# Kernel optimization log

Hardware: AMD Instinct MI355X
Metric: run time of the kernel (lower is better)

The kernel has to match this reference:

```python
import jax, jax.numpy as jnp
import numpy as np

KH, KW = 2, 2

def setup_inputs() -> dict:
    key = jax.random.key(0)
    k1, k2 = jax.random.split(key)
    x = jax.random.normal(k1, (64, 32, 32, 32), dtype=jnp.float32)
    # logits = log(rand) in torch; emulate with log of uniform to keep same distribution family
    logits = jnp.log(jax.random.uniform(k2, (32, 32, 32, 32), dtype=jnp.float32, minval=1e-6, maxval=1.0))
    return {"x": x, "logits": logits}


def reference(x, logits):
    # SumLayer: log_softmax over in_channels (dim=1), broadcast add, logsumexp over in
    log_w = jax.nn.log_softmax(logits, axis=1)            # [O, I, H, W]
    # x: [N, I, H, W] -> [N, 1, I, H, W]; log_w -> [1, O, I, H, W]
    y = jax.scipy.special.logsumexp(x[:, None] + log_w[None], axis=2)  # [N, O, H, W]
    # ProdConv: grouped conv with ones kernel, stride (KH,KW) == non-overlapping sum-pool
    N, C, H, W = y.shape
    y = y.reshape(N, C, H // KH, KH, W // KW, KW).sum(axis=(3, 5))     # [N, O, H/KH, W/KW]
    return y
```

## Files before the change

### kernel.cpp

```cpp
#include <hip/hip_runtime.h>

namespace {
constexpr int IC = 32;
constexpr int OC = 32;
constexpr int HW = 1024;
constexpr int H2 = 16, W2 = 16;

typedef _Float16 half2v __attribute__((ext_vector_type(2)));

#if defined(__has_builtin)
#if __has_builtin(__builtin_amdgcn_fdot2)
#define HAVE_FDOT2 1
#endif
#endif

__device__ __forceinline__ float dot2acc(half2v a, half2v b, float c) {
#ifdef HAVE_FDOT2
    return __builtin_amdgcn_fdot2(a, b, c, false);
#else
    return fmaf((float)a.x, (float)b.x, fmaf((float)a.y, (float)b.y, c));
#endif
}

__device__ __forceinline__ half2v u2h(unsigned int u) {
    union { unsigned int u; half2v h; } x; x.u = u; return x.h;
}

__device__ __forceinline__ half2v pk2(float a, float b) {
    union { decltype(__builtin_amdgcn_cvt_pkrtz(0.f, 0.f)) p; half2v h; } x;
    x.p = __builtin_amdgcn_cvt_pkrtz(a, b);
    return x.h;
}
}

__global__ __launch_bounds__(512, 4) void sumprod_fused(
    const float* __restrict__ x, const float* __restrict__ logits,
    float* __restrict__ out)
{
    __shared__ half2v exl[8 * 64 * 16];
    __shared__ half2v ewl[8 * 64 * 16];

    const int tid  = threadIdx.x;
    const int lane = tid & 63;
    const int w    = tid >> 6;
    const int bid  = blockIdx.x;
    const int s    = bid & 15;
    const int tt   = bid >> 4;
    const int n0   = (tt & 7) * 8;
    const int o0   = (tt >> 3) * 8;

    const int kk    = (tid >> 4) & 3;
    const int p4    = tid & 15;
    const int spoff = (2 * s + (p4 >> 3)) * 32 + (p4 & 7) * 4;

    const float* gx = x      + (size_t)(n0 + w) * IC * HW + spoff;
    const float* gw = logits + (size_t)(o0 + w) * IC * HW + spoff;

    auto stage = [&](half2v* buf, const float4& va, const float4& vb, int ip) {
        const float* pa = reinterpret_cast<const float*>(&va);
        const float* pb = reinterpret_cast<const float*>(&vb);
        #pragma unroll
        for (int j = 0; j < 4; ++j) {
            const int p    = (p4 >> 3) * 32 + (p4 & 7) * 4 + j;
            const int slot = (ip >> 2) ^ (((p >> 1) ^ (p >> 3)) & 3);
            buf[(w * 64 + p) * 16 + slot * 4 + (ip & 3)] =
                pk2(__expf(pa[j]), __expf(pb[j]));
        }
    };

    #pragma unroll
    for (int g = 0; g < 4; ++g) {
        const int ip = g * 4 + kk;
        const float4 va = *reinterpret_cast<const float4*>(&gw[(2 * ip) * HW]);
        const float4 vb = *reinterpret_cast<const float4*>(&gw[(2 * ip + 1) * HW]);
        stage(ewl, va, vb, ip);
    }
    #pragma unroll
    for (int g = 0; g < 4; ++g) {
        const int ip = g * 4 + kk;
        const float4 va = *reinterpret_cast<const float4*>(&gx[(2 * ip) * HW]);
        const float4 vb = *reinterpret_cast<const float4*>(&gx[(2 * ip + 1) * HW]);
        stage(exl, va, vb, ip);
    }
    __syncthreads();

    const int swl = ((lane >> 1) ^ (lane >> 3)) & 3;
    const int nw = (w & 1) * 4;
    const int ow = (w >> 1) * 2;

    const half2v one2 = {(_Float16)1.f, (_Float16)1.f};
    float den[2];
    #pragma unroll
    for (int j = 0; j < 2; ++j) {
        float ds = 0.f;
        const half2v* rb = &ewl[((ow + j) * 64 + lane) * 16];
        #pragma unroll
        for (int gg = 0; gg < 4; ++gg) {
            const uint4 B = *reinterpret_cast<const uint4*>(rb + ((gg ^ swl) * 4));
            ds = dot2acc(u2h(B.x), one2, ds);
            ds = dot2acc(u2h(B.y), one2, ds);
            ds = dot2acc(u2h(B.z), one2, ds);
            ds = dot2acc(u2h(B.w), one2, ds);
        }
        den[j] = ds;
    }

    float acc[4][2] = {};

#define D2(AA, BB, K, J) acc[K][J] = dot2acc(u2h(AA), u2h(BB), acc[K][J])
#define QUAD(A_, K_)                                                          \
    D2(A_.x, B0.x, K_, 0); D2(A_.y, B0.y, K_, 0);                             \
    D2(A_.z, B0.z, K_, 0); D2(A_.w, B0.w, K_, 0);                             \
    D2(A_.x, B1.x, K_, 1); D2(A_.y, B1.y, K_, 1);                             \
    D2(A_.z, B1.z, K_, 1); D2(A_.w, B1.w, K_, 1)
#define COMPUTE_GG(GG) {                                                      \
    const int off = ((GG) ^ swl) * 4;                                         \
    const uint4 A0 = *reinterpret_cast<const uint4*>(&exl[((nw + 0) * 64 + lane) * 16 + off]); \
    const uint4 A1 = *reinterpret_cast<const uint4*>(&exl[((nw + 1) * 64 + lane) * 16 + off]); \
    const uint4 A2 = *reinterpret_cast<const uint4*>(&exl[((nw + 2) * 64 + lane) * 16 + off]); \
    const uint4 A3 = *reinterpret_cast<const uint4*>(&exl[((nw + 3) * 64 + lane) * 16 + off]); \
    const uint4 B0 = *reinterpret_cast<const uint4*>(&ewl[((ow + 0) * 64 + lane) * 16 + off]); \
    const uint4 B1 = *reinterpret_cast<const uint4*>(&ewl[((ow + 1) * 64 + lane) * 16 + off]); \
    QUAD(A0, 0); QUAD(A1, 1); QUAD(A2, 2); QUAD(A3, 3); }

    COMPUTE_GG(0);
    COMPUTE_GG(1);
    COMPUTE_GG(2);
    COMPUTE_GG(3);

#undef COMPUTE_GG
#undef QUAD
#undef D2

    float dp0 = den[0];
    dp0 *= __shfl_xor(dp0, 1);  dp0 *= __shfl_xor(dp0, 32);
    float dp1 = den[1];
    dp1 *= __shfl_xor(dp1, 1);  dp1 *= __shfl_xor(dp1, 32);

    #pragma unroll
    for (int k = 0; k < 4; ++k) {
        #pragma unroll
        for (int j = 0; j < 2; ++j) {
            float v = acc[k][j];
            v *= __shfl_xor(v, 1);
            v *= __shfl_xor(v, 32);
            if ((lane & 33) == 0) {
                const int w2 = (lane >> 1) & 15;
                out[((n0 + nw + k) * OC + (o0 + ow + j)) * (H2 * W2) + s * W2 + w2] =
                    __logf(v) - __logf(j ? dp1 : dp0);
            }
        }
    }
}

extern "C" void kernel_launch(void* const* d_in, const int* in_sizes, int n_in,
                              void* d_out, int out_size, void* d_ws, size_t ws_size,
                              hipStream_t stream) {
    const float* x      = (const float*)d_in[0];
    const float* logits = (const float*)d_in[1];
    float* out = (float*)d_out;
    hipLaunchKernelGGL(sumprod_fused, dim3(512), dim3(512), 0, stream,
                       x, logits, out);
}
```

Baseline: 13.45 us.

## Halve block size, pipeline x staging across compute, compute denominators in fp32

```diff
diff --git a/kernel.cpp b/kernel.cpp
--- a/kernel.cpp
+++ b/kernel.cpp
@@ -26,23 +26,24 @@
     union { unsigned int u; half2v h; } x; x.u = u; return x.h;
 }
 
-__device__ __forceinline__ half2v pk2(float a, float b) {
-    union { decltype(__builtin_amdgcn_cvt_pkrtz(0.f, 0.f)) p; half2v h; } x;
+__device__ __forceinline__ unsigned int pk2u(float a, float b) {
+    union { decltype(__builtin_amdgcn_cvt_pkrtz(0.f, 0.f)) p; unsigned int u; } x;
     x.p = __builtin_amdgcn_cvt_pkrtz(a, b);
-    return x.h;
-}
-}
-
-__global__ __launch_bounds__(512, 4) void sumprod_fused(
+    return x.u;
+}
+}
+
+__global__ __launch_bounds__(256, 2) void sumprod_fused(
     const float* __restrict__ x, const float* __restrict__ logits,
     float* __restrict__ out)
 {
     __shared__ half2v exl[8 * 64 * 16];
     __shared__ half2v ewl[8 * 64 * 16];
+    __shared__ __align__(16) float wsl[8 * 64];
 
     const int tid  = threadIdx.x;
     const int lane = tid & 63;
-    const int w    = tid >> 6;
+    const int v    = tid >> 6;
     const int bid  = blockIdx.x;
     const int s    = bid & 15;
     const int tt   = bid >> 4;
@@ -51,68 +52,98 @@
 
     const int kk    = (tid >> 4) & 3;
     const int p4    = tid & 15;
-    const int spoff = (2 * s + (p4 >> 3)) * 32 + (p4 & 7) * 4;
-
-    const float* gx = x      + (size_t)(n0 + w) * IC * HW + spoff;
-    const float* gw = logits + (size_t)(o0 + w) * IC * HW + spoff;
-
-    auto stage = [&](half2v* buf, const float4& va, const float4& vb, int ip) {
-        const float* pa = reinterpret_cast<const float*>(&va);
-        const float* pb = reinterpret_cast<const float*>(&vb);
-        #pragma unroll
-        for (int j = 0; j < 4; ++j) {
-            const int p    = (p4 >> 3) * 32 + (p4 & 7) * 4 + j;
-            const int slot = (ip >> 2) ^ (((p >> 1) ^ (p >> 3)) & 3);
-            buf[(w * 64 + p) * 16 + slot * 4 + (ip & 3)] =
-                pk2(__expf(pa[j]), __expf(pb[j]));
-        }
-    };
-
-    #pragma unroll
-    for (int g = 0; g < 4; ++g) {
-        const int ip = g * 4 + kk;
-        const float4 va = *reinterpret_cast<const float4*>(&gw[(2 * ip) * HW]);
-        const float4 vb = *reinterpret_cast<const float4*>(&gw[(2 * ip + 1) * HW]);
-        stage(ewl, va, vb, ip);
-    }
-    #pragma unroll
-    for (int g = 0; g < 4; ++g) {
-        const int ip = g * 4 + kk;
-        const float4 va = *reinterpret_cast<const float4*>(&gx[(2 * ip) * HW]);
-        const float4 vb = *reinterpret_cast<const float4*>(&gx[(2 * ip + 1) * HW]);
-        stage(exl, va, vb, ip);
+    const int pbase = (p4 >> 3) * 32 + (p4 & 7) * 4;
+    const int spoff = 2 * s * 32 + pbase;
+
+    float dsum[2][4] = {};
+    #pragma unroll
+    for (int rr = 0; rr < 2; ++rr) {
+        const int r = v + rr * 4;
+        const float* g = logits + (size_t)(o0 + r) * IC * HW + spoff;
+        float4 va[4], vb[4];
+        #pragma unroll
+        for (int gi = 0; gi < 4; ++gi) {
+            const int ip = kk * 4 + gi;
+            va[gi] = *reinterpret_cast<const float4*>(&g[(2 * ip) * HW]);
+            vb[gi] = *reinterpret_cast<const float4*>(&g[(2 * ip + 1) * HW]);
+        }
+        #pragma unroll
+        for (int j = 0; j < 4; ++j) {
+            const int p    = pbase + j;
+            const int slot = kk ^ (((p >> 1) ^ (p >> 3)) & 3);
+            uint4 wv;
+            unsigned int* wp = &wv.x;
+            #pragma unroll
+            for (int gi = 0; gi < 4; ++gi) {
+                const float ea = __expf(reinterpret_cast<const float*>(&va[gi])[j]);
+                const float eb = __expf(reinterpret_cast<const float*>(&vb[gi])[j]);
+                dsum[rr][j] += ea + eb;
+                wp[gi] = pk2u(ea, eb);
+            }
+            *reinterpret_cast<uint4*>(&ewl[(r * 64 + p) * 16 + slot * 4]) = wv;
+        }
+    }
+    #pragma unroll
+    for (int rr = 0; rr < 2; ++rr) {
+        #pragma unroll
+        for (int j = 0; j < 4; ++j) {
+            float d = dsum[rr][j];
+            d += __shfl_xor(d, 16);
+            d += __shfl_xor(d, 32);
+            dsum[rr][j] = d;
+        }
+        if (kk == 0) {
+            float4 dv = make_float4(dsum[rr][0], dsum[rr][1], dsum[rr][2], dsum[rr][3]);
+            *reinterpret_cast<float4*>(&wsl[(v + rr * 4) * 64 + pbase]) = dv;
+        }
+    }
+
+    const float* gx0 = x + (size_t)(n0 + v) * IC * HW + spoff;
+    const float* gx1 = x + (size_t)(n0 + v + 4) * IC * HW + spoff;
+    #pragma unroll
+    for (int rr = 0; rr < 2; ++rr) {
+        const int r = v + rr * 4;
+        const float* gxr = rr ? gx1 : gx0;
+        float4 a0 = *reinterpret_cast<const float4*>(&gxr[(4 * kk + 0) * HW]);
+        float4 b0 = *reinterpret_cast<const float4*>(&gxr[(4 * kk + 1) * HW]);
+        float4 a1 = *reinterpret_cast<const float4*>(&gxr[(4 * kk + 2) * HW]);
+        float4 b1 = *reinterpret_cast<const float4*>(&gxr[(4 * kk + 3) * HW]);
+        #pragma unroll
+        for (int j = 0; j < 4; ++j) {
+            const int p    = pbase + j;
+            const int slot = (kk >> 1) ^ (((p >> 1) ^ (p >> 3)) & 3);
+            uint2 wv;
+            wv.x = pk2u(__expf(reinterpret_cast<const float*>(&a0)[j]),
+                        __expf(reinterpret_cast<const float*>(&b0)[j]));
+            wv.y = pk2u(__expf(reinterpret_cast<const float*>(&a1)[j]),
+                        __expf(reinterpret_cast<const float*>(&b1)[j]));
+            *reinterpret_cast<uint2*>(
+                &exl[(r * 64 + p) * 16 + slot * 4 + (kk & 1) * 2]) = wv;
+        }
     }
     __syncthreads();
 
+    float4 pf[2][4];
+    #pragma unroll
+    for (int rr = 0; rr < 2; ++rr) {
+        const float* gxr = rr ? gx1 : gx0;
+        pf[rr][0] = *reinterpret_cast<const float4*>(&gxr[(16 + 4 * kk + 0) * HW]);
+        pf[rr][1] = *reinterpret_cast<const float4*>(&gxr[(16 + 4 * kk + 1) * HW]);
+        pf[rr][2] = *reinterpret_cast<const float4*>(&gxr[(16 + 4 * kk + 2) * HW]);
+        pf[rr][3] = *reinterpret_cast<const float4*>(&gxr[(16 + 4 * kk + 3) * HW]);
+    }
+
     const int swl = ((lane >> 1) ^ (lane >> 3)) & 3;
-    const int nw = (w & 1) * 4;
-    const int ow = (w >> 1) * 2;
-
-    const half2v one2 = {(_Float16)1.f, (_Float16)1.f};
-    float den[2];
-    #pragma unroll
-    for (int j = 0; j < 2; ++j) {
-        float ds = 0.f;
-        const half2v* rb = &ewl[((ow + j) * 64 + lane) * 16];
-        #pragma unroll
-        for (int gg = 0; gg < 4; ++gg) {
-            const uint4 B = *reinterpret_cast<const uint4*>(rb + ((gg ^ swl) * 4));
-            ds = dot2acc(u2h(B.x), one2, ds);
-            ds = dot2acc(u2h(B.y), one2, ds);
-            ds = dot2acc(u2h(B.z), one2, ds);
-            ds = dot2acc(u2h(B.w), one2, ds);
-        }
-        den[j] = ds;
-    }
-
-    float acc[4][2] = {};
+    const int nw = (v & 1) * 4;
+    const int ow = (v >> 1) * 4;
+    float acc[4][4] = {};
 
 #define D2(AA, BB, K, J) acc[K][J] = dot2acc(u2h(AA), u2h(BB), acc[K][J])
-#define QUAD(A_, K_)                                                          \
-    D2(A_.x, B0.x, K_, 0); D2(A_.y, B0.y, K_, 0);                             \
-    D2(A_.z, B0.z, K_, 0); D2(A_.w, B0.w, K_, 0);                             \
-    D2(A_.x, B1.x, K_, 1); D2(A_.y, B1.y, K_, 1);                             \
-    D2(A_.z, B1.z, K_, 1); D2(A_.w, B1.w, K_, 1)
+#define OCT(A_, K_)                                                           \
+    D2(A_.x, B0.x, K_, 0); D2(A_.y, B0.y, K_, 0); D2(A_.z, B0.z, K_, 0); D2(A_.w, B0.w, K_, 0); \
+    D2(A_.x, B1.x, K_, 1); D2(A_.y, B1.y, K_, 1); D2(A_.z, B1.z, K_, 1); D2(A_.w, B1.w, K_, 1); \
+    D2(A_.x, B2.x, K_, 2); D2(A_.y, B2.y, K_, 2); D2(A_.z, B2.z, K_, 2); D2(A_.w, B2.w, K_, 2); \
+    D2(A_.x, B3.x, K_, 3); D2(A_.y, B3.y, K_, 3); D2(A_.z, B3.z, K_, 3); D2(A_.w, B3.w, K_, 3)
 #define COMPUTE_GG(GG) {                                                      \
     const int off = ((GG) ^ swl) * 4;                                         \
     const uint4 A0 = *reinterpret_cast<const uint4*>(&exl[((nw + 0) * 64 + lane) * 16 + off]); \
@@ -121,33 +152,53 @@
     const uint4 A3 = *reinterpret_cast<const uint4*>(&exl[((nw + 3) * 64 + lane) * 16 + off]); \
     const uint4 B0 = *reinterpret_cast<const uint4*>(&ewl[((ow + 0) * 64 + lane) * 16 + off]); \
     const uint4 B1 = *reinterpret_cast<const uint4*>(&ewl[((ow + 1) * 64 + lane) * 16 + off]); \
-    QUAD(A0, 0); QUAD(A1, 1); QUAD(A2, 2); QUAD(A3, 3); }
+    const uint4 B2 = *reinterpret_cast<const uint4*>(&ewl[((ow + 2) * 64 + lane) * 16 + off]); \
+    const uint4 B3 = *reinterpret_cast<const uint4*>(&ewl[((ow + 3) * 64 + lane) * 16 + off]); \
+    OCT(A0, 0); OCT(A1, 1); OCT(A2, 2); OCT(A3, 3); }
 
     COMPUTE_GG(0);
     COMPUTE_GG(1);
+
+    #pragma unroll
+    for (int rr = 0; rr < 2; ++rr) {
+        const int r = v + rr * 4;
+        #pragma unroll
+        for (int j = 0; j < 4; ++j) {
+            const int p    = pbase + j;
+            const int slot = (2 + (kk >> 1)) ^ (((p >> 1) ^ (p >> 3)) & 3);
+            uint2 wv;
+            wv.x = pk2u(__expf(reinterpret_cast<const float*>(&pf[rr][0])[j]),
+                        __expf(reinterpret_cast<const float*>(&pf[rr][1])[j]));
+            wv.y = pk2u(__expf(reinterpret_cast<const float*>(&pf[rr][2])[j]),
+                        __expf(reinterpret_cast<const float*>(&pf[rr][3])[j]));
+            *reinterpret_cast<uint2*>(
+                &exl[(r * 64 + p) * 16 + slot * 4 + (kk & 1) * 2]) = wv;
+        }
+    }
+    __syncthreads();
+
     COMPUTE_GG(2);
     COMPUTE_GG(3);
 
 #undef COMPUTE_GG
-#undef QUAD
+#undef OCT
 #undef D2
 
-    float dp0 = den[0];
-    dp0 *= __shfl_xor(dp0, 1);  dp0 *= __shfl_xor(dp0, 32);
-    float dp1 = den[1];
-    dp1 *= __shfl_xor(dp1, 1);  dp1 *= __shfl_xor(dp1, 32);
+    float lw[4];
+    #pragma unroll
+    for (int jj = 0; jj < 4; ++jj)
+        lw[jj] = __logf(wsl[(ow + jj) * 64 + lane]);
 
     #pragma unroll
     for (int k = 0; k < 4; ++k) {
         #pragma unroll
-        for (int j = 0; j < 2; ++j) {
-            float v = acc[k][j];
-            v *= __shfl_xor(v, 1);
-            v *= __shfl_xor(v, 32);
+        for (int jj = 0; jj < 4; ++jj) {
+            float val = __logf(acc[k][jj]) - lw[jj];
+            val += __shfl_xor(val, 1);
+            val += __shfl_xor(val, 32);
             if ((lane & 33) == 0) {
                 const int w2 = (lane >> 1) & 15;
-                out[((n0 + nw + k) * OC + (o0 + ow + j)) * (H2 * W2) + s * W2 + w2] =
-                    __logf(v) - __logf(j ? dp1 : dp0);
+                out[((n0 + nw + k) * OC + (o0 + ow + jj)) * (H2 * W2) + s * W2 + w2] = val;
             }
         }
     }
@@ -159,6 +210,6 @@
     const float* x      = (const float*)d_in[0];
     const float* logits = (const float*)d_in[1];
     float* out = (float*)d_out;
-    hipLaunchKernelGGL(sumprod_fused, dim3(512), dim3(512), 0, stream,
+    hipLaunchKernelGGL(sumprod_fused, dim3(512), dim3(256), 0, stream,
                        x, logits, out);
 }
```

After: 13.79 us. 2.5% more time.
